# Optimization experiments

Measured on AMD Instinct MI355X. Metric: run time of the kernel, lower is better.

The kernel has to match this reference:

```python
import jax, jax.numpy as jnp
import numpy as np

RADIUS = 3
SIGMA = 2.0
T_STEPS = 30


def _gauss_kernel():
    i = jnp.arange(-RADIUS, RADIUS + 1, dtype=jnp.float32)
    w = jnp.exp(-0.5 * (i / SIGMA) ** 2)
    return w / w.sum()


def _gauss_axis(x, w, axis):
    # scipy mode='reflect' == numpy pad mode='symmetric'
    pad = [(0, 0)] * x.ndim
    pad[axis] = (RADIUS, RADIUS)
    xp = jnp.pad(x, pad, mode='symmetric')
    n = x.shape[axis]
    out = w[0] * jax.lax.slice_in_dim(xp, 0, n, axis=axis)
    for k in range(1, 2 * RADIUS + 1):
        out = out + w[k] * jax.lax.slice_in_dim(xp, k, k + n, axis=axis)
    return out


def _dog(x):
    # scipy gaussian_filter with scalar sigma filters EVERY axis (incl. batch, channel).
    # sigma2=0 axis filters are skipped by scipy -> blurred2 == x.
    w = _gauss_kernel()
    g = x
    for ax in range(x.ndim):
        g = _gauss_axis(g, w, ax)
    return jnp.abs(g - x)


def _conv(x, w):
    return jax.lax.conv_general_dilated(
        x, w, window_strides=(1, 1), padding='VALID',
        dimension_numbers=('NCHW', 'OIHW', 'NCHW'))


def _maxpool2(x, pad):
    return jax.lax.reduce_window(
        x, -jnp.inf, jax.lax.max, (1, 1, 2, 2), (1, 1, 2, 2),
        [(0, 0), (0, 0), (pad, pad), (pad, pad)])


def setup_inputs() -> dict:
    key = jax.random.key(0)
    kx, k1, k2, k3 = jax.random.split(key, 4)
    x = jax.random.uniform(kx, (4096, 1, 28, 28), dtype=jnp.float32)
    # model constructor takes abs() of all conv weights
    w1 = jnp.abs(jax.random.normal(k1, (4, 1, 3, 3), dtype=jnp.float32) / 3.0)
    w2 = jnp.abs(jax.random.normal(k2, (4, 4, 3, 3), dtype=jnp.float32) / 6.0)
    w3 = jnp.abs(jax.random.normal(k3, (1, 4, 3, 3), dtype=jnp.float32) / 6.0)
    return {'x': x, 'w1': w1, 'w2': w2, 'w3': w3}


def reference(x, w1, w2, w3):
    x = x.reshape(-1, 1, 28, 28)
    n = x.shape[0]
    dt = x.dtype
    # DoG preproc + global-max normalization (input is constant across timesteps,
    # so computing it once is mathematically identical to the per-step recompute)
    d = _dog(x)
    d = d / d.max()

    def step(carry, _):
        v1, v2, v3, v4, pred = carry
        # IFNode(4.5): integrate, fire, hard reset to 0
        v1 = v1 + d
        s1 = (v1 >= 4.5).astype(dt)
        v1 = jnp.where(s1 > 0, 0.0, v1)
        # conv1 -> IFNode(4.5) -> maxpool2
        v2 = v2 + _conv(s1, w1)                 # [n,4,26,26]
        s2 = (v2 >= 4.5).astype(dt)
        v2 = jnp.where(s2 > 0, 0.0, v2)
        p1 = _maxpool2(s2, 0)                   # [n,4,13,13]
        # conv2 -> IFNode(1.0) -> maxpool2(pad=1)
        v3 = v3 + _conv(p1, w2)                 # [n,4,11,11]
        s3 = (v3 >= 1.0).astype(dt)
        v3 = jnp.where(s3 > 0, 0.0, v3)
        p2 = _maxpool2(s3, 1)                   # [n,4,6,6]
        # conv3 -> LIFNode(tau=2, v_th=1.0, decay_input=True, hard reset)
        c3 = _conv(p2, w3)                      # [n,1,4,4]
        v4 = v4 + (c3 - v4) / 2.0
        s4 = (v4 >= 1.0).astype(dt)
        v4 = jnp.where(s4 > 0, 0.0, v4)
        return (v1, v2, v3, v4, pred + s4), None

    z = lambda s: jnp.zeros(s, dt)
    carry0 = (z((n, 1, 28, 28)), z((n, 4, 26, 26)), z((n, 4, 11, 11)),
              z((n, 1, 4, 4)), z((n, 1, 4, 4)))
    (v1, v2, v3, v4, pred), _ = jax.lax.scan(step, carry0, None, length=T_STEPS)
    return (pred / T_STEPS).reshape(-1, 4, 4)
```

## Files before the change

### kernel.cpp

```cpp
#include <hip/hip_runtime.h>
#include <math.h>

#define HW 784
#define TSTEPS 30

struct GaussW { float w[7]; };

__device__ __forceinline__ float fadd(float a, float b) { return __fadd_rn(a, b); }
__device__ __forceinline__ float fmul(float a, float b) { return __fmul_rn(a, b); }
__device__ __forceinline__ float fsub(float a, float b) { return __fsub_rn(a, b); }

#if defined(__has_builtin)
#  if __has_builtin(__builtin_amdgcn_ubfe)
#    define UBFE(x, o, w) __builtin_amdgcn_ubfe((unsigned)(x), (unsigned)(o), (unsigned)(w))
#  endif
#endif
#ifndef UBFE
#  define UBFE(x, o, w) (((unsigned)(x) >> (o)) & ((1u << (w)) - 1u))
#endif

#define WFENCE() asm volatile("s_waitcnt lgkmcnt(0)" ::: "memory")

__device__ __forceinline__ int refl(int i, int n) {
    if (i < 0) return -i - 1;
    if (i >= n) return 2 * n - 1 - i;
    return i;
}

__device__ void dog_sample(const float* __restrict__ x, int b, int nbatch,
                           const GaussW gw, float* g, float* t,
                           float* dout, int tid) {
    for (int p = tid; p < HW; p += 256) {
        float acc = fmul(gw.w[0], x[(size_t)refl(b - 3, nbatch) * HW + p]);
        #pragma unroll
        for (int k = 1; k < 7; ++k)
            acc = fadd(acc, fmul(gw.w[k], x[(size_t)refl(b - 3 + k, nbatch) * HW + p]));
        float h = fmul(gw.w[0], acc);
        #pragma unroll
        for (int k = 1; k < 7; ++k)
            h = fadd(h, fmul(gw.w[k], acc));
        g[p] = h;
    }
    __syncthreads();
    for (int p = tid; p < HW; p += 256) {
        int i = p / 28, j = p - (p / 28) * 28;
        float acc = fmul(gw.w[0], g[refl(i - 3, 28) * 28 + j]);
        #pragma unroll
        for (int k = 1; k < 7; ++k)
            acc = fadd(acc, fmul(gw.w[k], g[refl(i - 3 + k, 28) * 28 + j]));
        t[p] = acc;
    }
    __syncthreads();
    for (int p = tid; p < HW; p += 256) {
        int i = p / 28, j = p - (p / 28) * 28;
        float acc = fmul(gw.w[0], t[i * 28 + refl(j - 3, 28)]);
        #pragma unroll
        for (int k = 1; k < 7; ++k)
            acc = fadd(acc, fmul(gw.w[k], t[i * 28 + refl(j - 3 + k, 28)]));
        dout[p] = fabsf(fsub(acc, x[(size_t)b * HW + p]));
    }
    __syncthreads();
}

__global__ void init_kernel(unsigned int* dmax) { *dmax = 0u; }

template<bool CACHE>
__global__ __launch_bounds__(256) void dmax_kernel(const float* __restrict__ x,
                                                   int nbatch, GaussW gw,
                                                   unsigned int* __restrict__ dmax,
                                                   float* __restrict__ dcache) {
    __shared__ float gS[4][HW];
    __shared__ float tS[4][HW];
    int tid = threadIdx.x;
    int lane = tid & 63, wv = tid >> 6;
    int b = blockIdx.x * 4 + wv;
    int bs = b < nbatch ? b : nbatch - 1;
    float* g = gS[wv];
    float* t = tS[wv];
    const float* xb = x + (size_t)bs * HW;
    const float* xr[7];
    #pragma unroll
    for (int k = 0; k < 7; ++k)
        xr[k] = x + (size_t)refl(bs - 3 + k, nbatch) * HW;

    for (int r = 0; r < 13; ++r) {
        int p = (r << 6) + lane;
        if (p < HW) {
            float acc = fmul(gw.w[0], xr[0][p]);
            #pragma unroll
            for (int k = 1; k < 7; ++k)
                acc = fadd(acc, fmul(gw.w[k], xr[k][p]));
            float h = fmul(gw.w[0], acc);
            #pragma unroll
            for (int k = 1; k < 7; ++k)
                h = fadd(h, fmul(gw.w[k], acc));
            g[p] = h;
        }
    }
    WFENCE();
    for (int r = 0; r < 13; ++r) {
        int p = (r << 6) + lane;
        if (p < HW) {
            int i = p / 28, j = p - (p / 28) * 28;
            float acc = fmul(gw.w[0], g[refl(i - 3, 28) * 28 + j]);
            #pragma unroll
            for (int k = 1; k < 7; ++k)
                acc = fadd(acc, fmul(gw.w[k], g[refl(i - 3 + k, 28) * 28 + j]));
            t[p] = acc;
        }
    }
    WFENCE();
    float mx = 0.f;
    for (int r = 0; r < 13; ++r) {
        int p = (r << 6) + lane;
        if (p < HW) {
            int i = p / 28, j = p - (p / 28) * 28;
            float acc = fmul(gw.w[0], t[i * 28 + refl(j - 3, 28)]);
            #pragma unroll
            for (int k = 1; k < 7; ++k)
                acc = fadd(acc, fmul(gw.w[k], t[i * 28 + refl(j - 3 + k, 28)]));
            float d = fabsf(fsub(acc, xb[p]));
            if (CACHE) dcache[(size_t)bs * HW + p] = d;
            mx = fmaxf(mx, d);
        }
    }
    #pragma unroll
    for (int off = 32; off; off >>= 1) mx = fmaxf(mx, __shfl_down(mx, off, 64));
    if (lane == 0) atomicMax(dmax, __float_as_uint(mx));
}

template<bool CACHE>
__global__ __launch_bounds__(256, 6) void sim_kernel(const float* __restrict__ x,
        int nbatch,
        const float* __restrict__ w1g, const float* __restrict__ w2g,
        const float* __restrict__ w3g, GaussW gw,
        const unsigned int* __restrict__ dmaxp,
        const float* __restrict__ dcache,
        float* __restrict__ out) {
    __shared__ __align__(16) float4 lut[512];
    __shared__ __align__(8)  float2 lut2[768];
    __shared__ float lut3[96];
    __shared__ float wts[216];
    __shared__ unsigned s1m[TSTEPS * 28];
    __shared__ __align__(8) unsigned p1p[TSTEPS * 26];
    __shared__ unsigned p2p[TSTEPS * 6];

    int tid = threadIdx.x;
    int lane = tid & 63, wv = tid >> 6;
    int b = blockIdx.x;
    if (b >= nbatch) b = nbatch - 1;

    if (tid < 36)  wts[tid]       = w1g[tid];
    if (tid < 144) wts[36 + tid]  = w2g[tid];
    if (tid < 36)  wts[180 + tid] = w3g[tid];

    float dmaxv = __uint_as_float(*dmaxp);
    float dnr[4];
    if (CACHE) {
        const float* dcb = dcache + (size_t)b * HW;
        #pragma unroll
        for (int k = 0; k < 4; ++k) {
            int r = wv + 4 * k;
            int p = 56 * r + (lane < 56 ? lane : 0);
            float d = (r < 14) ? dcb[p] : 0.f;
            dnr[k] = (lane < 56 && r < 14) ? __fdiv_rn(d, dmaxv) : 0.f;
        }
    } else {
        float* scr = (float*)lut;
        dog_sample(x, b, nbatch, gw, scr, scr + HW, scr, tid);
        #pragma unroll
        for (int k = 0; k < 4; ++k) {
            int r = wv + 4 * k;
            int p = 56 * r + (lane < 56 ? lane : 0);
            float d = (r < 14) ? scr[p] : 0.f;
            dnr[k] = (lane < 56 && r < 14) ? __fdiv_rn(d, dmaxv) : 0.f;
        }
    }
    __syncthreads();

    for (int e = tid; e < 512; e += 256) {
        float a0 = 0.f, a1 = 0.f, a2 = 0.f, a3 = 0.f;
        #pragma unroll
        for (int k = 0; k < 9; ++k) {
            bool bit = (e >> k) & 1;
            a0 = fadd(a0, bit ? wts[k]      : 0.0f);
            a1 = fadd(a1, bit ? wts[9 + k]  : 0.0f);
            a2 = fadd(a2, bit ? wts[18 + k] : 0.0f);
            a3 = fadd(a3, bit ? wts[27 + k] : 0.0f);
        }
        lut[e] = make_float4(a0, a1, a2, a3);
    }
    for (int e = tid; e < 768; e += 256) {
        int rowIdx = e >> 4, idx = e & 15;
        int cout = rowIdx / 12, rem = rowIdx - cout * 12;
        int ic = rem / 3, ki = rem - ic * 3;
        const float* wb = &wts[36 + cout * 36 + ic * 9 + ki * 3];
        float xx = 0.f, yy = 0.f;
        #pragma unroll
        for (int kk = 0; kk < 3; ++kk) {
            xx = fadd(xx, ((idx >> kk) & 1) ? wb[kk] : 0.0f);
            yy = fadd(yy, ((idx >> (kk + 1)) & 1) ? wb[kk] : 0.0f);
        }
        lut2[e] = make_float2(xx, yy);
    }
    if (tid < 96) {
        int ric = tid >> 3, idx = tid & 7;
        int ic = ric / 3, ki = ric - ic * 3;
        const float* wb = &wts[180 + ic * 9 + ki * 3];
        float xx = 0.f;
        #pragma unroll
        for (int kk = 0; kk < 3; ++kk)
            xx = fadd(xx, ((idx >> kk) & 1) ? wb[kk] : 0.0f);
        lut3[tid] = xx;
    }
    #pragma unroll
    for (int j = 0; j < 8; ++j) {
        int idx = tid + (j << 8);
        if (idx < TSTEPS * 60) {
            if (idx < TSTEPS * 28) s1m[idx] = 0u;
            else if (idx < TSTEPS * 54) p1p[idx - TSTEPS * 28] = 0u;
            else p2p[idx - TSTEPS * 54] = 0u;
        }
    }
    __syncthreads();

    bool okq = tid < 169;
    int qq1 = okq ? tid : 0;
    int pi1 = qq1 / 13, pj1 = qq1 - pi1 * 13;
    int sr1 = 2 * pi1; unsigned sh1 = (unsigned)(2 * pj1);
    unsigned pb1 = 1u << (pj1 + 1);
    bool hasB = tid >= 248;
    int i2A, lbA, pwA; unsigned jsA, shA, bA0, bA1;
    int i2B, lbB, pwB; unsigned jsB, shB, bB0, bB1;
    {
        int m = tid;
        int row = m / 6, sub = m - row * 6;
        int j0 = (sub < 5) ? 2 * sub : 10;
        int c = row / 11, i2 = row - c * 11;
        i2A = i2; jsA = (unsigned)(j0 + 1); lbA = c * 192; shA = 6u * (unsigned)c;
        pwA = (i2 + 1) >> 1;
        bA0 = 1u << (j0 >> 1);
        bA1 = (sub < 5) ? (2u << (j0 >> 1)) : 0u;
        m = hasB ? 256 + (tid - 248) : 0;
        row = m / 6; sub = m - row * 6;
        j0 = (sub < 5) ? 2 * sub : 10;
        c = row / 11; i2 = row - c * 11;
        i2B = i2; jsB = (unsigned)(j0 + 1); lbB = c * 192; shB = 6u * (unsigned)c;
        pwB = (i2 + 1) >> 1;
        bB0 = 1u << (j0 >> 1);
        bB1 = (sub < 5) ? (2u << (j0 >> 1)) : 0u;
    }
    int rr3 = (tid >> 2) & 3, cc3 = tid & 3;

    float v2q[16] = {};
    float v3A[2] = {0.f, 0.f}, v3B[2] = {0.f, 0.f};
    float v1m[4] = {};
    float v4 = 0.f, pred = 0.f;

    #pragma unroll 1
    for (int tt = 0; tt < TSTEPS; ++tt) {
        unsigned* s1 = s1m + tt * 28;
        #pragma unroll
        for (int k = 0; k < 4; ++k) {
            if (k < 3 || wv < 2) {
                int r = wv + 4 * k;
                float v = fadd(v1m[k], dnr[k]);
                bool spk = (lane < 56) && (v >= 4.5f);
                v1m[k] = spk ? 0.f : v;
                unsigned long long bal = __ballot(spk);
                if (lane < 2)
                    s1[2 * r + lane] = (unsigned)(lane ? (bal >> 28) : bal) & 0x0FFFFFFFu;
            }
        }
    }
    __syncthreads();

    if (okq) {
        #pragma unroll 1
        for (int tt = 0; tt < TSTEPS; ++tt) {
            const unsigned* s1 = s1m + tt * 28;
            unsigned m0 = s1[sr1], m1 = s1[sr1 + 1], m2 = s1[sr1 + 2], m3 = s1[sr1 + 3];
            unsigned a = UBFE(m0, sh1, 4), bq = UBFE(m1, sh1, 4),
                     cq = UBFE(m2, sh1, 4), dq = UBFE(m3, sh1, 4);
            unsigned a7 = a & 7u, b7 = bq & 7u, c7 = cq & 7u, d7 = dq & 7u;
            unsigned a1 = a >> 1, b1 = bq >> 1, c1 = cq >> 1, d1 = dq >> 1;
            unsigned p00 = a7 | (b7 << 3) | (c7 << 6);
            unsigned p01 = a1 | (b1 << 3) | (c1 << 6);
            unsigned p10 = b7 | (c7 << 3) | (d7 << 6);
            unsigned p11 = b1 | (c1 << 3) | (d1 << 6);
            float4 e00 = lut[p00], e01 = lut[p01], e10 = lut[p10], e11 = lut[p11];
            unsigned cb0 = 0, cb1 = 0, cb2 = 0, cb3 = 0;
            #define C1U(E, ci) { float v; bool s; \
                v = fadd(v2q[(ci)*4+0], E.x); s = v>=4.5f; v2q[(ci)*4+0] = s?0.f:v; cb0 |= (unsigned)s; \
                v = fadd(v2q[(ci)*4+1], E.y); s = v>=4.5f; v2q[(ci)*4+1] = s?0.f:v; cb1 |= (unsigned)s; \
                v = fadd(v2q[(ci)*4+2], E.z); s = v>=4.5f; v2q[(ci)*4+2] = s?0.f:v; cb2 |= (unsigned)s; \
                v = fadd(v2q[(ci)*4+3], E.w); s = v>=4.5f; v2q[(ci)*4+3] = s?0.f:v; cb3 |= (unsigned)s; }
            C1U(e00, 0) C1U(e01, 1) C1U(e10, 2) C1U(e11, 3)
            #undef C1U
            unsigned* pw = &p1p[(tt * 13 + pi1) * 2];
            unsigned orm0 = (cb0 ? pb1 : 0u) | (cb1 ? (pb1 << 16) : 0u);
            unsigned orm1 = (cb2 ? pb1 : 0u) | (cb3 ? (pb1 << 16) : 0u);
            if (orm0) atomicOr(&pw[0], orm0);
            if (orm1) atomicOr(&pw[1], orm1);
        }
    }
    __syncthreads();

    #pragma unroll 1
    for (int tt = 0; tt < TSTEPS; ++tt) {
        const uint2* pp = (const uint2*)&p1p[tt * 26];
        unsigned* p2w = &p2p[tt * 6];
        {
            uint2 r0 = pp[i2A], r1 = pp[i2A + 1], r2 = pp[i2A + 2];
            float accA = 0.f, accB = 0.f;
            #pragma unroll
            for (int ic = 0; ic < 4; ++ic) {
                unsigned rw0 = (ic < 2) ? r0.x : r0.y;
                unsigned rw1 = (ic < 2) ? r1.x : r1.y;
                unsigned rw2 = (ic < 2) ? r2.x : r2.y;
                unsigned fo = jsA + ((unsigned)(ic & 1) << 4);
                #pragma unroll
                for (int ki = 0; ki < 3; ++ki) {
                    unsigned row = (ki == 0) ? rw0 : (ki == 1) ? rw1 : rw2;
                    unsigned idx = UBFE(row, fo, 4);
                    float2 e = lut2[lbA + (ic * 3 + ki) * 16 + idx];
                    accA = fadd(accA, e.x);
                    accB = fadd(accB, e.y);
                }
            }
            float va = fadd(v3A[0], accA);
            float vb = fadd(v3A[1], accB);
            bool sa = va >= 1.0f, sb = vb >= 1.0f;
            v3A[0] = sa ? 0.f : va; v3A[1] = sb ? 0.f : vb;
            unsigned orm = (sa ? bA0 : 0u) | (sb ? bA1 : 0u);
            if (orm) atomicOr(&p2w[pwA], orm << shA);
        }
        if (hasB) {
            uint2 r0 = pp[i2B], r1 = pp[i2B + 1], r2 = pp[i2B + 2];
            float accA = 0.f, accB = 0.f;
            #pragma unroll
            for (int ic = 0; ic < 4; ++ic) {
                unsigned rw0 = (ic < 2) ? r0.x : r0.y;
                unsigned rw1 = (ic < 2) ? r1.x : r1.y;
                unsigned rw2 = (ic < 2) ? r2.x : r2.y;
                unsigned fo = jsB + ((unsigned)(ic & 1) << 4);
                #pragma unroll
                for (int ki = 0; ki < 3; ++ki) {
                    unsigned row = (ki == 0) ? rw0 : (ki == 1) ? rw1 : rw2;
                    unsigned idx = UBFE(row, fo, 4);
                    float2 e = lut2[lbB + (ic * 3 + ki) * 16 + idx];
                    accA = fadd(accA, e.x);
                    accB = fadd(accB, e.y);
                }
            }
            float va = fadd(v3B[0], accA);
            float vb = fadd(v3B[1], accB);
            bool sa = va >= 1.0f, sb = vb >= 1.0f;
            v3B[0] = sa ? 0.f : va; v3B[1] = sb ? 0.f : vb;
            unsigned orm = (sa ? bB0 : 0u) | (sb ? bB1 : 0u);
            if (orm) atomicOr(&p2w[pwB], orm << shB);
        }
    }
    __syncthreads();

    if (tid < 16) {
        #pragma unroll 1
        for (int tt = 0; tt < TSTEPS; ++tt) {
            const unsigned* p2 = &p2p[tt * 6];
            unsigned r0 = p2[rr3], r1 = p2[rr3 + 1], r2 = p2[rr3 + 2];
            float acc = 0.f;
            #pragma unroll
            for (int ic = 0; ic < 4; ++ic) {
                #pragma unroll
                for (int ki = 0; ki < 3; ++ki) {
                    unsigned row = (ki == 0) ? r0 : (ki == 1) ? r1 : r2;
                    unsigned idx = UBFE(row, 6 * ic + cc3, 3);
                    acc = fadd(acc, lut3[(ic * 3 + ki) * 8 + idx]);
                }
            }
            v4 = fadd(v4, fmul(fsub(acc, v4), 0.5f));
            if (v4 >= 1.0f) { pred += 1.f; v4 = 0.f; }
        }
        if (blockIdx.x < (unsigned)nbatch)
            out[(size_t)blockIdx.x * 16 + tid] = __fdiv_rn(pred, 30.0f);
    }
}

extern "C" void kernel_launch(void* const* d_in, const int* in_sizes, int n_in,
                              void* d_out, int out_size, void* d_ws, size_t ws_size,
                              hipStream_t stream) {
    const float* x  = (const float*)d_in[0];
    const float* w1 = (const float*)d_in[1];
    const float* w2 = (const float*)d_in[2];
    const float* w3 = (const float*)d_in[3];
    float* out = (float*)d_out;
    unsigned int* dmax = (unsigned int*)d_ws;
    float* dcache = (float*)((char*)d_ws + 16);

    int nbatch = in_sizes[0] / HW;
    size_t need = 16 + (size_t)nbatch * HW * sizeof(float);
    bool cache = ws_size >= need;
    int g4 = (nbatch + 3) / 4;

    GaussW gw;
    {
        float fw[7];
        for (int k = 0; k < 7; ++k) {
            float iv = (float)(k - 3);
            float q = iv / 2.0f;
            float e = -0.5f * (q * q);
            fw[k] = (float)exp((double)e);
        }
        float s = 0.0f;
        for (int k = 0; k < 7; ++k) s += fw[k];
        for (int k = 0; k < 7; ++k) gw.w[k] = fw[k] / s;
    }

    hipLaunchKernelGGL(init_kernel, dim3(1), dim3(1), 0, stream, dmax);
    if (cache) {
        hipLaunchKernelGGL(dmax_kernel<true>, dim3(g4), dim3(256), 0, stream,
                           x, nbatch, gw, dmax, dcache);
        hipLaunchKernelGGL(sim_kernel<true>, dim3(nbatch), dim3(256), 0, stream,
                           x, nbatch, w1, w2, w3, gw, dmax, dcache, out);
    } else {
        hipLaunchKernelGGL(dmax_kernel<false>, dim3(g4), dim3(256), 0, stream,
                           x, nbatch, gw, dmax, dcache);
        hipLaunchKernelGGL(sim_kernel<false>, dim3(nbatch), dim3(256), 0, stream,
                           x, nbatch, w1, w2, w3, gw, dmax, dcache, out);
    }
}
```

Measured before the change: 230.6 us.

## Rebalance conv2 work across threads and parallelize conv3 over timesteps

```diff
diff --git a/kernel.cpp b/kernel.cpp
--- a/kernel.cpp
+++ b/kernel.cpp
@@ -61,8 +61,6 @@
     }
     __syncthreads();
 }
-
-__global__ void init_kernel(unsigned int* dmax) { *dmax = 0u; }
 
 template<bool CACHE>
 __global__ __launch_bounds__(256) void dmax_kernel(const float* __restrict__ x,
@@ -144,6 +142,7 @@
     __shared__ unsigned s1m[TSTEPS * 28];
     __shared__ __align__(8) unsigned p1p[TSTEPS * 26];
     __shared__ unsigned p2p[TSTEPS * 6];
+    __shared__ float accb[TSTEPS * 16];
 
     int tid = threadIdx.x;
     int lane = tid & 63, wv = tid >> 6;
@@ -229,33 +228,29 @@
     int pi1 = qq1 / 13, pj1 = qq1 - pi1 * 13;
     int sr1 = 2 * pi1; unsigned sh1 = (unsigned)(2 * pj1);
     unsigned pb1 = 1u << (pj1 + 1);
-    bool hasB = tid >= 248;
-    int i2A, lbA, pwA; unsigned jsA, shA, bA0, bA1;
-    int i2B, lbB, pwB; unsigned jsB, shB, bB0, bB1;
+    int c2, i2, jp0, ncell2;
     {
-        int m = tid;
-        int row = m / 6, sub = m - row * 6;
-        int j0 = (sub < 5) ? 2 * sub : 10;
-        int c = row / 11, i2 = row - c * 11;
-        i2A = i2; jsA = (unsigned)(j0 + 1); lbA = c * 192; shA = 6u * (unsigned)c;
-        pwA = (i2 + 1) >> 1;
-        bA0 = 1u << (j0 >> 1);
-        bA1 = (sub < 5) ? (2u << (j0 >> 1)) : 0u;
-        m = hasB ? 256 + (tid - 248) : 0;
-        row = m / 6; sub = m - row * 6;
-        j0 = (sub < 5) ? 2 * sub : 10;
-        c = row / 11; i2 = row - c * 11;
-        i2B = i2; jsB = (unsigned)(j0 + 1); lbB = c * 192; shB = 6u * (unsigned)c;
-        pwB = (i2 + 1) >> 1;
-        bB0 = 1u << (j0 >> 1);
-        bB1 = (sub < 5) ? (2u << (j0 >> 1)) : 0u;
-    }
-    int rr3 = (tid >> 2) & 3, cc3 = tid & 3;
+        int rowid, sub;
+        if (tid < 216) {
+            rowid = tid / 6; sub = tid - rowid * 6;
+            jp0 = (sub < 5) ? 2 * sub : 10; ncell2 = (sub < 5) ? 2 : 1;
+        } else {
+            int u = tid - 216; int r5 = u / 5; sub = u - r5 * 5;
+            rowid = 36 + r5;
+            jp0 = (sub < 4) ? 2 * sub : 8; ncell2 = (sub < 4) ? 2 : 3;
+        }
+        c2 = rowid / 11; i2 = rowid - c2 * 11;
+    }
+    unsigned js2 = (unsigned)(jp0 + 1);
+    int lb2 = c2 * 192;
+    unsigned sh6 = 6u * (unsigned)c2;
+    int pw2 = (i2 + 1) >> 1;
+    unsigned b20 = 1u << (jp0 >> 1);
+    unsigned b21 = 2u << (jp0 >> 1);
 
     float v2q[16] = {};
-    float v3A[2] = {0.f, 0.f}, v3B[2] = {0.f, 0.f};
+    float v3m[3] = {0.f, 0.f, 0.f};
     float v1m[4] = {};
-    float v4 = 0.f, pred = 0.f;
 
     #pragma unroll 1
     for (int tt = 0; tt < TSTEPS; ++tt) {
@@ -310,74 +305,70 @@
     for (int tt = 0; tt < TSTEPS; ++tt) {
         const uint2* pp = (const uint2*)&p1p[tt * 26];
         unsigned* p2w = &p2p[tt * 6];
-        {
-            uint2 r0 = pp[i2A], r1 = pp[i2A + 1], r2 = pp[i2A + 2];
-            float accA = 0.f, accB = 0.f;
-            #pragma unroll
-            for (int ic = 0; ic < 4; ++ic) {
-                unsigned rw0 = (ic < 2) ? r0.x : r0.y;
-                unsigned rw1 = (ic < 2) ? r1.x : r1.y;
-                unsigned rw2 = (ic < 2) ? r2.x : r2.y;
-                unsigned fo = jsA + ((unsigned)(ic & 1) << 4);
-                #pragma unroll
-                for (int ki = 0; ki < 3; ++ki) {
-                    unsigned row = (ki == 0) ? rw0 : (ki == 1) ? rw1 : rw2;
-                    unsigned idx = UBFE(row, fo, 4);
-                    float2 e = lut2[lbA + (ic * 3 + ki) * 16 + idx];
-                    accA = fadd(accA, e.x);
-                    accB = fadd(accB, e.y);
+        uint2 r0 = pp[i2], r1 = pp[i2 + 1], r2 = pp[i2 + 2];
+        float a0 = 0.f, a1 = 0.f, a2c = 0.f;
+        #pragma unroll
+        for (int ic = 0; ic < 4; ++ic) {
+            unsigned rw0 = (ic < 2) ? r0.x : r0.y;
+            unsigned rw1 = (ic < 2) ? r1.x : r1.y;
+            unsigned rw2 = (ic < 2) ? r2.x : r2.y;
+            unsigned fo = js2 + ((unsigned)(ic & 1) << 4);
+            #pragma unroll
+            for (int ki = 0; ki < 3; ++ki) {
+                unsigned row = (ki == 0) ? rw0 : (ki == 1) ? rw1 : rw2;
+                unsigned idx = UBFE(row, fo, 4);
+                float2 e = lut2[lb2 + (ic * 3 + ki) * 16 + idx];
+                a0 = fadd(a0, e.x);
+                a1 = fadd(a1, e.y);
+                if (ncell2 == 3) {
+                    unsigned idx2 = UBFE(row, fo + 2, 4);
+                    a2c = fadd(a2c, lut2[lb2 + (ic * 3 + ki) * 16 + idx2].x);
                 }
             }
-            float va = fadd(v3A[0], accA);
-            float vb = fadd(v3A[1], accB);
-            bool sa = va >= 1.0f, sb = vb >= 1.0f;
-            v3A[0] = sa ? 0.f : va; v3A[1] = sb ? 0.f : vb;
-            unsigned orm = (sa ? bA0 : 0u) | (sb ? bA1 : 0u);
-            if (orm) atomicOr(&p2w[pwA], orm << shA);
-        }
-        if (hasB) {
-            uint2 r0 = pp[i2B], r1 = pp[i2B + 1], r2 = pp[i2B + 2];
-            float accA = 0.f, accB = 0.f;
-            #pragma unroll
-            for (int ic = 0; ic < 4; ++ic) {
-                unsigned rw0 = (ic < 2) ? r0.x : r0.y;
-                unsigned rw1 = (ic < 2) ? r1.x : r1.y;
-                unsigned rw2 = (ic < 2) ? r2.x : r2.y;
-                unsigned fo = jsB + ((unsigned)(ic & 1) << 4);
-                #pragma unroll
-                for (int ki = 0; ki < 3; ++ki) {
-                    unsigned row = (ki == 0) ? rw0 : (ki == 1) ? rw1 : rw2;
-                    unsigned idx = UBFE(row, fo, 4);
-                    float2 e = lut2[lbB + (ic * 3 + ki) * 16 + idx];
-                    accA = fadd(accA, e.x);
-                    accB = fadd(accB, e.y);
-                }
+        }
+        unsigned orm = 0u;
+        { float v = fadd(v3m[0], a0); bool s = v >= 1.0f;
+          v3m[0] = s ? 0.f : v; if (s) orm |= b20; }
+        if (ncell2 >= 2) {
+            float v = fadd(v3m[1], a1); bool s = v >= 1.0f;
+            v3m[1] = s ? 0.f : v; if (s) orm |= b21;
+            if (ncell2 == 3) {
+                float v2 = fadd(v3m[2], a2c); bool s2 = v2 >= 1.0f;
+                v3m[2] = s2 ? 0.f : v2; if (s2) orm |= b21;
             }
-            float va = fadd(v3B[0], accA);
-            float vb = fadd(v3B[1], accB);
-            bool sa = va >= 1.0f, sb = vb >= 1.0f;
-            v3B[0] = sa ? 0.f : va; v3B[1] = sb ? 0.f : vb;
-            unsigned orm = (sa ? bB0 : 0u) | (sb ? bB1 : 0u);
-            if (orm) atomicOr(&p2w[pwB], orm << shB);
-        }
-    }
-    __syncthreads();
-
-    if (tid < 16) {
-        #pragma unroll 1
-        for (int tt = 0; tt < TSTEPS; ++tt) {
+        }
+        if (orm) atomicOr(&p2w[pw2], orm << sh6);
+    }
+    __syncthreads();
+
+    #pragma unroll
+    for (int h = 0; h < 2; ++h) {
+        int m = tid + (h << 8);
+        if (m < TSTEPS * 16) {
+            int tt = m >> 4, cell = m & 15;
+            int rr = cell >> 2, cc = cell & 3;
             const unsigned* p2 = &p2p[tt * 6];
-            unsigned r0 = p2[rr3], r1 = p2[rr3 + 1], r2 = p2[rr3 + 2];
+            unsigned r0 = p2[rr], r1 = p2[rr + 1], r2 = p2[rr + 2];
             float acc = 0.f;
             #pragma unroll
             for (int ic = 0; ic < 4; ++ic) {
                 #pragma unroll
                 for (int ki = 0; ki < 3; ++ki) {
                     unsigned row = (ki == 0) ? r0 : (ki == 1) ? r1 : r2;
-                    unsigned idx = UBFE(row, 6 * ic + cc3, 3);
+                    unsigned idx = UBFE(row, 6 * ic + cc, 3);
                     acc = fadd(acc, lut3[(ic * 3 + ki) * 8 + idx]);
                 }
             }
+            accb[m] = acc;
+        }
+    }
+    __syncthreads();
+
+    if (tid < 16) {
+        float v4 = 0.f, pred = 0.f;
+        #pragma unroll 1
+        for (int tt = 0; tt < TSTEPS; ++tt) {
+            float acc = accb[tt * 16 + tid];
             v4 = fadd(v4, fmul(fsub(acc, v4), 0.5f));
             if (v4 >= 1.0f) { pred += 1.f; v4 = 0.f; }
         }
@@ -416,7 +407,7 @@
         for (int k = 0; k < 7; ++k) gw.w[k] = fw[k] / s;
     }
 
-    hipLaunchKernelGGL(init_kernel, dim3(1), dim3(1), 0, stream, dmax);
+    hipMemsetAsync(dmax, 0, 4, stream);
     if (cache) {
         hipLaunchKernelGGL(dmax_kernel<true>, dim3(g4), dim3(256), 0, stream,
                            x, nbatch, gw, dmax, dcache);
```

Measured after the change: 237.3 us. 2.9% more time.

## Process two samples per sim block and replace init kernel with memset

Applied to the files above, without the earlier changes.

```diff
diff --git a/kernel.cpp b/kernel.cpp
--- a/kernel.cpp
+++ b/kernel.cpp
@@ -61,8 +61,6 @@
     }
     __syncthreads();
 }
-
-__global__ void init_kernel(unsigned int* dmax) { *dmax = 0u; }
 
 template<bool CACHE>
 __global__ __launch_bounds__(256) void dmax_kernel(const float* __restrict__ x,
@@ -147,33 +145,47 @@
 
     int tid = threadIdx.x;
     int lane = tid & 63, wv = tid >> 6;
-    int b = blockIdx.x;
-    if (b >= nbatch) b = nbatch - 1;
+    int bA = blockIdx.x * 2;
+    int bB = bA + 1;
+    int bAc = bA < nbatch ? bA : nbatch - 1;
+    int bBc = bB < nbatch ? bB : nbatch - 1;
 
     if (tid < 36)  wts[tid]       = w1g[tid];
     if (tid < 144) wts[36 + tid]  = w2g[tid];
     if (tid < 36)  wts[180 + tid] = w3g[tid];
 
     float dmaxv = __uint_as_float(*dmaxp);
-    float dnr[4];
+    float dnrA[4], dnrB[4];
     if (CACHE) {
-        const float* dcb = dcache + (size_t)b * HW;
+        const float* da = dcache + (size_t)bAc * HW;
+        const float* db = dcache + (size_t)bBc * HW;
         #pragma unroll
         for (int k = 0; k < 4; ++k) {
             int r = wv + 4 * k;
             int p = 56 * r + (lane < 56 ? lane : 0);
-            float d = (r < 14) ? dcb[p] : 0.f;
-            dnr[k] = (lane < 56 && r < 14) ? __fdiv_rn(d, dmaxv) : 0.f;
+            bool ok = (lane < 56 && r < 14);
+            int pc = (r < 14) ? p : 0;
+            dnrA[k] = ok ? __fdiv_rn(da[pc], dmaxv) : 0.f;
+            dnrB[k] = ok ? __fdiv_rn(db[pc], dmaxv) : 0.f;
         }
     } else {
         float* scr = (float*)lut;
-        dog_sample(x, b, nbatch, gw, scr, scr + HW, scr, tid);
+        dog_sample(x, bAc, nbatch, gw, scr, scr + HW, scr, tid);
         #pragma unroll
         for (int k = 0; k < 4; ++k) {
             int r = wv + 4 * k;
             int p = 56 * r + (lane < 56 ? lane : 0);
             float d = (r < 14) ? scr[p] : 0.f;
-            dnr[k] = (lane < 56 && r < 14) ? __fdiv_rn(d, dmaxv) : 0.f;
+            dnrA[k] = (lane < 56 && r < 14) ? __fdiv_rn(d, dmaxv) : 0.f;
+        }
+        __syncthreads();
+        dog_sample(x, bBc, nbatch, gw, scr, scr + HW, scr, tid);
+        #pragma unroll
+        for (int k = 0; k < 4; ++k) {
+            int r = wv + 4 * k;
+            int p = 56 * r + (lane < 56 ? lane : 0);
+            float d = (r < 14) ? scr[p] : 0.f;
+            dnrB[k] = (lane < 56 && r < 14) ? __fdiv_rn(d, dmaxv) : 0.f;
         }
     }
     __syncthreads();
@@ -229,7 +241,7 @@
     int pi1 = qq1 / 13, pj1 = qq1 - pi1 * 13;
     int sr1 = 2 * pi1; unsigned sh1 = (unsigned)(2 * pj1);
     unsigned pb1 = 1u << (pj1 + 1);
-    bool hasB = tid >= 248;
+    bool hasB2 = tid >= 248;
     int i2A, lbA, pwA; unsigned jsA, shA, bA0, bA1;
     int i2B, lbB, pwB; unsigned jsB, shB, bB0, bB1;
     {
@@ -241,7 +253,7 @@
         pwA = (i2 + 1) >> 1;
         bA0 = 1u << (j0 >> 1);
         bA1 = (sub < 5) ? (2u << (j0 >> 1)) : 0u;
-        m = hasB ? 256 + (tid - 248) : 0;
+        m = hasB2 ? 256 + (tid - 248) : 0;
         row = m / 6; sub = m - row * 6;
         j0 = (sub < 5) ? 2 * sub : 10;
         c = row / 11; i2 = row - c * 11;
@@ -252,137 +264,157 @@
     }
     int rr3 = (tid >> 2) & 3, cc3 = tid & 3;
 
-    float v2q[16] = {};
-    float v3A[2] = {0.f, 0.f}, v3B[2] = {0.f, 0.f};
-    float v1m[4] = {};
-    float v4 = 0.f, pred = 0.f;
-
-    #pragma unroll 1
-    for (int tt = 0; tt < TSTEPS; ++tt) {
-        unsigned* s1 = s1m + tt * 28;
-        #pragma unroll
-        for (int k = 0; k < 4; ++k) {
-            if (k < 3 || wv < 2) {
-                int r = wv + 4 * k;
-                float v = fadd(v1m[k], dnr[k]);
-                bool spk = (lane < 56) && (v >= 4.5f);
-                v1m[k] = spk ? 0.f : v;
-                unsigned long long bal = __ballot(spk);
-                if (lane < 2)
-                    s1[2 * r + lane] = (unsigned)(lane ? (bal >> 28) : bal) & 0x0FFFFFFFu;
-            }
-        }
-    }
-    __syncthreads();
-
-    if (okq) {
+    #pragma unroll
+    for (int s = 0; s < 2; ++s) {
+        float v2q[16] = {};
+        float v3A[2] = {0.f, 0.f}, v3B[2] = {0.f, 0.f};
+        float v1m[4] = {};
+        float v4 = 0.f, pred = 0.f;
+
+        if (s == 1 && lane >= 56) {
+            int base = wv * 8 + (lane - 56);
+            #pragma unroll
+            for (int j = 0; j < 6; ++j) {
+                int idx = base + 32 * j;
+                if (idx < TSTEPS * 6) p2p[idx] = 0u;
+            }
+        }
         #pragma unroll 1
         for (int tt = 0; tt < TSTEPS; ++tt) {
-            const unsigned* s1 = s1m + tt * 28;
-            unsigned m0 = s1[sr1], m1 = s1[sr1 + 1], m2 = s1[sr1 + 2], m3 = s1[sr1 + 3];
-            unsigned a = UBFE(m0, sh1, 4), bq = UBFE(m1, sh1, 4),
-                     cq = UBFE(m2, sh1, 4), dq = UBFE(m3, sh1, 4);
-            unsigned a7 = a & 7u, b7 = bq & 7u, c7 = cq & 7u, d7 = dq & 7u;
-            unsigned a1 = a >> 1, b1 = bq >> 1, c1 = cq >> 1, d1 = dq >> 1;
-            unsigned p00 = a7 | (b7 << 3) | (c7 << 6);
-            unsigned p01 = a1 | (b1 << 3) | (c1 << 6);
-            unsigned p10 = b7 | (c7 << 3) | (d7 << 6);
-            unsigned p11 = b1 | (c1 << 3) | (d1 << 6);
-            float4 e00 = lut[p00], e01 = lut[p01], e10 = lut[p10], e11 = lut[p11];
-            unsigned cb0 = 0, cb1 = 0, cb2 = 0, cb3 = 0;
-            #define C1U(E, ci) { float v; bool s; \
-                v = fadd(v2q[(ci)*4+0], E.x); s = v>=4.5f; v2q[(ci)*4+0] = s?0.f:v; cb0 |= (unsigned)s; \
-                v = fadd(v2q[(ci)*4+1], E.y); s = v>=4.5f; v2q[(ci)*4+1] = s?0.f:v; cb1 |= (unsigned)s; \
-                v = fadd(v2q[(ci)*4+2], E.z); s = v>=4.5f; v2q[(ci)*4+2] = s?0.f:v; cb2 |= (unsigned)s; \
-                v = fadd(v2q[(ci)*4+3], E.w); s = v>=4.5f; v2q[(ci)*4+3] = s?0.f:v; cb3 |= (unsigned)s; }
-            C1U(e00, 0) C1U(e01, 1) C1U(e10, 2) C1U(e11, 3)
-            #undef C1U
-            unsigned* pw = &p1p[(tt * 13 + pi1) * 2];
-            unsigned orm0 = (cb0 ? pb1 : 0u) | (cb1 ? (pb1 << 16) : 0u);
-            unsigned orm1 = (cb2 ? pb1 : 0u) | (cb3 ? (pb1 << 16) : 0u);
-            if (orm0) atomicOr(&pw[0], orm0);
-            if (orm1) atomicOr(&pw[1], orm1);
-        }
-    }
-    __syncthreads();
-
-    #pragma unroll 1
-    for (int tt = 0; tt < TSTEPS; ++tt) {
-        const uint2* pp = (const uint2*)&p1p[tt * 26];
-        unsigned* p2w = &p2p[tt * 6];
-        {
-            uint2 r0 = pp[i2A], r1 = pp[i2A + 1], r2 = pp[i2A + 2];
-            float accA = 0.f, accB = 0.f;
-            #pragma unroll
-            for (int ic = 0; ic < 4; ++ic) {
-                unsigned rw0 = (ic < 2) ? r0.x : r0.y;
-                unsigned rw1 = (ic < 2) ? r1.x : r1.y;
-                unsigned rw2 = (ic < 2) ? r2.x : r2.y;
-                unsigned fo = jsA + ((unsigned)(ic & 1) << 4);
-                #pragma unroll
-                for (int ki = 0; ki < 3; ++ki) {
-                    unsigned row = (ki == 0) ? rw0 : (ki == 1) ? rw1 : rw2;
-                    unsigned idx = UBFE(row, fo, 4);
-                    float2 e = lut2[lbA + (ic * 3 + ki) * 16 + idx];
-                    accA = fadd(accA, e.x);
-                    accB = fadd(accB, e.y);
+            unsigned* s1 = s1m + tt * 28;
+            #pragma unroll
+            for (int k = 0; k < 4; ++k) {
+                if (k < 3 || wv < 2) {
+                    int r = wv + 4 * k;
+                    float dv = (s == 0) ? dnrA[k] : dnrB[k];
+                    float v = fadd(v1m[k], dv);
+                    bool spk = (lane < 56) && (v >= 4.5f);
+                    v1m[k] = spk ? 0.f : v;
+                    unsigned long long bal = __ballot(spk);
+                    if (lane < 2)
+                        s1[2 * r + lane] = (unsigned)(lane ? (bal >> 28) : bal) & 0x0FFFFFFFu;
                 }
             }
-            float va = fadd(v3A[0], accA);
-            float vb = fadd(v3A[1], accB);
-            bool sa = va >= 1.0f, sb = vb >= 1.0f;
-            v3A[0] = sa ? 0.f : va; v3A[1] = sb ? 0.f : vb;
-            unsigned orm = (sa ? bA0 : 0u) | (sb ? bA1 : 0u);
-            if (orm) atomicOr(&p2w[pwA], orm << shA);
-        }
-        if (hasB) {
-            uint2 r0 = pp[i2B], r1 = pp[i2B + 1], r2 = pp[i2B + 2];
-            float accA = 0.f, accB = 0.f;
-            #pragma unroll
-            for (int ic = 0; ic < 4; ++ic) {
-                unsigned rw0 = (ic < 2) ? r0.x : r0.y;
-                unsigned rw1 = (ic < 2) ? r1.x : r1.y;
-                unsigned rw2 = (ic < 2) ? r2.x : r2.y;
-                unsigned fo = jsB + ((unsigned)(ic & 1) << 4);
-                #pragma unroll
-                for (int ki = 0; ki < 3; ++ki) {
-                    unsigned row = (ki == 0) ? rw0 : (ki == 1) ? rw1 : rw2;
-                    unsigned idx = UBFE(row, fo, 4);
-                    float2 e = lut2[lbB + (ic * 3 + ki) * 16 + idx];
-                    accA = fadd(accA, e.x);
-                    accB = fadd(accB, e.y);
-                }
-            }
-            float va = fadd(v3B[0], accA);
-            float vb = fadd(v3B[1], accB);
-            bool sa = va >= 1.0f, sb = vb >= 1.0f;
-            v3B[0] = sa ? 0.f : va; v3B[1] = sb ? 0.f : vb;
-            unsigned orm = (sa ? bB0 : 0u) | (sb ? bB1 : 0u);
-            if (orm) atomicOr(&p2w[pwB], orm << shB);
-        }
-    }
-    __syncthreads();
-
-    if (tid < 16) {
+        }
+        __syncthreads();
+
+        if (okq) {
+            #pragma unroll 1
+            for (int tt = 0; tt < TSTEPS; ++tt) {
+                const unsigned* s1 = s1m + tt * 28;
+                unsigned m0 = s1[sr1], m1 = s1[sr1 + 1], m2 = s1[sr1 + 2], m3 = s1[sr1 + 3];
+                unsigned a = UBFE(m0, sh1, 4), bq = UBFE(m1, sh1, 4),
+                         cq = UBFE(m2, sh1, 4), dq = UBFE(m3, sh1, 4);
+                unsigned a7 = a & 7u, b7 = bq & 7u, c7 = cq & 7u, d7 = dq & 7u;
+                unsigned a1 = a >> 1, b1 = bq >> 1, c1 = cq >> 1, d1 = dq >> 1;
+                unsigned p00 = a7 | (b7 << 3) | (c7 << 6);
+                unsigned p01 = a1 | (b1 << 3) | (c1 << 6);
+                unsigned p10 = b7 | (c7 << 3) | (d7 << 6);
+                unsigned p11 = b1 | (c1 << 3) | (d1 << 6);
+                float4 e00 = lut[p00], e01 = lut[p01], e10 = lut[p10], e11 = lut[p11];
+                unsigned cb0 = 0, cb1 = 0, cb2 = 0, cb3 = 0;
+                #define C1U(E, ci) { float v; bool sx; \
+                    v = fadd(v2q[(ci)*4+0], E.x); sx = v>=4.5f; v2q[(ci)*4+0] = sx?0.f:v; cb0 |= (unsigned)sx; \
+                    v = fadd(v2q[(ci)*4+1], E.y); sx = v>=4.5f; v2q[(ci)*4+1] = sx?0.f:v; cb1 |= (unsigned)sx; \
+                    v = fadd(v2q[(ci)*4+2], E.z); sx = v>=4.5f; v2q[(ci)*4+2] = sx?0.f:v; cb2 |= (unsigned)sx; \
+                    v = fadd(v2q[(ci)*4+3], E.w); sx = v>=4.5f; v2q[(ci)*4+3] = sx?0.f:v; cb3 |= (unsigned)sx; }
+                C1U(e00, 0) C1U(e01, 1) C1U(e10, 2) C1U(e11, 3)
+                #undef C1U
+                unsigned* pw = &p1p[(tt * 13 + pi1) * 2];
+                unsigned orm0 = (cb0 ? pb1 : 0u) | (cb1 ? (pb1 << 16) : 0u);
+                unsigned orm1 = (cb2 ? pb1 : 0u) | (cb3 ? (pb1 << 16) : 0u);
+                if (orm0) atomicOr(&pw[0], orm0);
+                if (orm1) atomicOr(&pw[1], orm1);
+            }
+        }
+        __syncthreads();
+
         #pragma unroll 1
         for (int tt = 0; tt < TSTEPS; ++tt) {
-            const unsigned* p2 = &p2p[tt * 6];
-            unsigned r0 = p2[rr3], r1 = p2[rr3 + 1], r2 = p2[rr3 + 2];
-            float acc = 0.f;
-            #pragma unroll
-            for (int ic = 0; ic < 4; ++ic) {
+            const uint2* pp = (const uint2*)&p1p[tt * 26];
+            unsigned* p2w = &p2p[tt * 6];
+            {
+                uint2 r0 = pp[i2A], r1 = pp[i2A + 1], r2 = pp[i2A + 2];
+                float accA = 0.f, accB = 0.f;
                 #pragma unroll
-                for (int ki = 0; ki < 3; ++ki) {
-                    unsigned row = (ki == 0) ? r0 : (ki == 1) ? r1 : r2;
-                    unsigned idx = UBFE(row, 6 * ic + cc3, 3);
-                    acc = fadd(acc, lut3[(ic * 3 + ki) * 8 + idx]);
+                for (int ic = 0; ic < 4; ++ic) {
+                    unsigned rw0 = (ic < 2) ? r0.x : r0.y;
+                    unsigned rw1 = (ic < 2) ? r1.x : r1.y;
+                    unsigned rw2 = (ic < 2) ? r2.x : r2.y;
+                    unsigned fo = jsA + ((unsigned)(ic & 1) << 4);
+                    #pragma unroll
+                    for (int ki = 0; ki < 3; ++ki) {
+                        unsigned row = (ki == 0) ? rw0 : (ki == 1) ? rw1 : rw2;
+                        unsigned idx = UBFE(row, fo, 4);
+                        float2 e = lut2[lbA + (ic * 3 + ki) * 16 + idx];
+                        accA = fadd(accA, e.x);
+                        accB = fadd(accB, e.y);
+                    }
                 }
-            }
-            v4 = fadd(v4, fmul(fsub(acc, v4), 0.5f));
-            if (v4 >= 1.0f) { pred += 1.f; v4 = 0.f; }
-        }
-        if (blockIdx.x < (unsigned)nbatch)
-            out[(size_t)blockIdx.x * 16 + tid] = __fdiv_rn(pred, 30.0f);
+                float va = fadd(v3A[0], accA);
+                float vb = fadd(v3A[1], accB);
+                bool sa = va >= 1.0f, sb = vb >= 1.0f;
+                v3A[0] = sa ? 0.f : va; v3A[1] = sb ? 0.f : vb;
+                unsigned orm = (sa ? bA0 : 0u) | (sb ? bA1 : 0u);
+                if (orm) atomicOr(&p2w[pwA], orm << shA);
+            }
+            if (hasB2) {
+                uint2 r0 = pp[i2B], r1 = pp[i2B + 1], r2 = pp[i2B + 2];
+                float accA = 0.f, accB = 0.f;
+                #pragma unroll
+                for (int ic = 0; ic < 4; ++ic) {
+                    unsigned rw0 = (ic < 2) ? r0.x : r0.y;
+                    unsigned rw1 = (ic < 2) ? r1.x : r1.y;
+                    unsigned rw2 = (ic < 2) ? r2.x : r2.y;
+                    unsigned fo = jsB + ((unsigned)(ic & 1) << 4);
+                    #pragma unroll
+                    for (int ki = 0; ki < 3; ++ki) {
+                        unsigned row = (ki == 0) ? rw0 : (ki == 1) ? rw1 : rw2;
+                        unsigned idx = UBFE(row, fo, 4);
+                        float2 e = lut2[lbB + (ic * 3 + ki) * 16 + idx];
+                        accA = fadd(accA, e.x);
+                        accB = fadd(accB, e.y);
+                    }
+                }
+                float va = fadd(v3B[0], accA);
+                float vb = fadd(v3B[1], accB);
+                bool sa = va >= 1.0f, sb = vb >= 1.0f;
+                v3B[0] = sa ? 0.f : va; v3B[1] = sb ? 0.f : vb;
+                unsigned orm = (sa ? bB0 : 0u) | (sb ? bB1 : 0u);
+                if (orm) atomicOr(&p2w[pwB], orm << shB);
+            }
+        }
+        __syncthreads();
+
+        if (tid < 16) {
+            #pragma unroll 1
+            for (int tt = 0; tt < TSTEPS; ++tt) {
+                const unsigned* p2 = &p2p[tt * 6];
+                unsigned r0 = p2[rr3], r1 = p2[rr3 + 1], r2 = p2[rr3 + 2];
+                float acc = 0.f;
+                #pragma unroll
+                for (int ic = 0; ic < 4; ++ic) {
+                    #pragma unroll
+                    for (int ki = 0; ki < 3; ++ki) {
+                        unsigned row = (ki == 0) ? r0 : (ki == 1) ? r1 : r2;
+                        unsigned idx = UBFE(row, 6 * ic + cc3, 3);
+                        acc = fadd(acc, lut3[(ic * 3 + ki) * 8 + idx]);
+                    }
+                }
+                v4 = fadd(v4, fmul(fsub(acc, v4), 0.5f));
+                if (v4 >= 1.0f) { pred += 1.f; v4 = 0.f; }
+            }
+            int bs = (s == 0) ? bA : bB;
+            if (bs < nbatch)
+                out[(size_t)bs * 16 + tid] = __fdiv_rn(pred, 30.0f);
+        } else if (s == 0) {
+            #pragma unroll
+            for (int j = 0; j < 4; ++j) {
+                int idx = (tid - 16) + 240 * j;
+                if (idx < TSTEPS * 26) p1p[idx] = 0u;
+            }
+        }
+        __syncthreads();
     }
 }
 
@@ -401,6 +433,7 @@
     size_t need = 16 + (size_t)nbatch * HW * sizeof(float);
     bool cache = ws_size >= need;
     int g4 = (nbatch + 3) / 4;
+    int g2 = (nbatch + 1) / 2;
 
     GaussW gw;
     {
@@ -416,16 +449,16 @@
         for (int k = 0; k < 7; ++k) gw.w[k] = fw[k] / s;
     }
 
-    hipLaunchKernelGGL(init_kernel, dim3(1), dim3(1), 0, stream, dmax);
+    hipMemsetAsync(dmax, 0, 4, stream);
     if (cache) {
         hipLaunchKernelGGL(dmax_kernel<true>, dim3(g4), dim3(256), 0, stream,
                            x, nbatch, gw, dmax, dcache);
-        hipLaunchKernelGGL(sim_kernel<true>, dim3(nbatch), dim3(256), 0, stream,
+        hipLaunchKernelGGL(sim_kernel<true>, dim3(g2), dim3(256), 0, stream,
                            x, nbatch, w1, w2, w3, gw, dmax, dcache, out);
     } else {
         hipLaunchKernelGGL(dmax_kernel<false>, dim3(g4), dim3(256), 0, stream,
                            x, nbatch, gw, dmax, dcache);
-        hipLaunchKernelGGL(sim_kernel<false>, dim3(nbatch), dim3(256), 0, stream,
+        hipLaunchKernelGGL(sim_kernel<false>, dim3(g2), dim3(256), 0, stream,
                            x, nbatch, w1, w2, w3, gw, dmax, dcache, out);
     }
 }
```

New measurement: 254.0 us. 1.1x slower.
